# Kernel tuning notes

Hardware: AMD Instinct MI355X
Metric: run time of the kernel (lower is better)

Reference implementation:

```python
import jax, jax.numpy as jnp
import numpy as np

B, S, H = 2, 2048, 4096
NH, NKV, D = 32, 8, 128  # heads, kv heads, head_dim


def rotate_half(x):
    x1, x2 = jnp.split(x, 2, axis=-1)
    return jnp.concatenate((-x2, x1), axis=-1)


def setup_inputs() -> dict:
    key = jax.random.key(0)
    ks = jax.random.split(key, 5)
    hidden_states = jax.random.normal(ks[0], (B, S, H), jnp.float32) * 0.02
    wq = jax.random.normal(ks[1], (H, NH * D), jnp.float32) * 0.02
    wk = jax.random.normal(ks[2], (H, NKV * D), jnp.float32) * 0.02
    wv = jax.random.normal(ks[3], (H, NKV * D), jnp.float32) * 0.02
    wo = jax.random.normal(ks[4], (NH * D, H), jnp.float32) * 0.02
    # Llama rotary cache: emb = cat(freqs, freqs); cos/sin shape [S, D]
    inv_freq = 1.0 / (10000.0 ** (jnp.arange(0, D, 2, dtype=jnp.float32) / D))
    t = jnp.arange(S, dtype=jnp.float32)
    freqs = jnp.einsum('i,j->ij', t, inv_freq)
    emb = jnp.concatenate((freqs, freqs), axis=-1)
    cos, sin = jnp.cos(emb), jnp.sin(emb)
    # additive causal mask [S, S]
    causal = jnp.tril(jnp.ones((S, S), dtype=bool))
    attn_mask = jnp.where(causal, 0.0, -1e9).astype(jnp.float32)
    return {'hidden_states': hidden_states, 'wq': wq, 'wk': wk, 'wv': wv,
            'wo': wo, 'cos': cos, 'sin': sin, 'attn_mask': attn_mask}


def reference(hidden_states, wq, wk, wv, wo, cos, sin, attn_mask):
    b, s, _ = hidden_states.shape
    q = (hidden_states @ wq).reshape(b, s, NH, D)   # [b,s,nh,d]
    k = (hidden_states @ wk).reshape(b, s, NKV, D)  # [b,s,nkv,d]
    v = (hidden_states @ wv).reshape(b, s, NKV, D)
    c = cos[None, :, None, :]  # [1,s,1,d]
    sn = sin[None, :, None, :]
    q = q * c + rotate_half(q) * sn
    k = k * c + rotate_half(k) * sn
    # GQA: repeat KV heads to match query heads
    grp = NH // NKV
    k = jnp.repeat(k, grp, axis=2)
    v = jnp.repeat(v, grp, axis=2)
    scale = 1.0 / np.sqrt(D).astype(np.float32)
    scores = jnp.einsum('bqhd,bkhd->bhqk', q, k) * scale
    scores = scores + attn_mask[None, None, :, :]
    probs = jax.nn.softmax(scores, axis=-1)
    out = jnp.einsum('bhqk,bkhd->bqhd', probs, v).reshape(b, s, NH * D)
    return out @ wo
```

## Files before the change

kernel.cpp:

```cpp
#include <hip/hip_runtime.h>

typedef __attribute__((ext_vector_type(8))) short short8;
typedef __attribute__((ext_vector_type(4))) float f32x4;
typedef __attribute__((ext_vector_type(4))) int int4v;

__device__ __forceinline__ float bf2f(unsigned short u) {
  unsigned int x = ((unsigned int)u) << 16;
  float f;
  __builtin_memcpy(&f, &x, 4);
  return f;
}
__device__ __forceinline__ unsigned short f2bf(float f) {
  unsigned int x;
  __builtin_memcpy(&x, &f, 4);
  unsigned int r = (x + 0x7FFFu + ((x >> 16) & 1u)) >> 16;
  return (unsigned short)r;
}
__device__ __forceinline__ unsigned int cvtpk_bf16(float lo, float hi) {
  unsigned int r;
  asm("v_cvt_pk_bf16_f32 %0, %1, %2" : "=v"(r) : "v"(lo), "v"(hi));
  return r;
}
__device__ __forceinline__ int4v s8_to_i4(short8 v) {
  int4v r;
  __builtin_memcpy(&r, &v, 16);
  return r;
}
__device__ __forceinline__ short8 i4_to_s8(int4v v) {
  short8 r;
  __builtin_memcpy(&r, &v, 16);
  return r;
}
__device__ __forceinline__ short8 ld8_f32(const float* p) {
  f32x4 x = *(const f32x4*)p;
  f32x4 y = *(const f32x4*)(p + 4);
  short8 r;
  r[0] = (short)f2bf(x[0]); r[1] = (short)f2bf(x[1]);
  r[2] = (short)f2bf(x[2]); r[3] = (short)f2bf(x[3]);
  r[4] = (short)f2bf(y[0]); r[5] = (short)f2bf(y[1]);
  r[6] = (short)f2bf(y[2]); r[7] = (short)f2bf(y[3]);
  return r;
}

__device__ __forceinline__ void async16(unsigned short* lds, const unsigned short* g) {
  __builtin_amdgcn_global_load_lds(
      (const __attribute__((address_space(1))) void*)g,
      (__attribute__((address_space(3))) void*)lds, 16, 0, 0);
}

__global__ void downcast_f2b(const float* __restrict__ in,
                             unsigned short* __restrict__ out, int n8) {
  int i = blockIdx.x * 256 + threadIdx.x;
  if (i >= n8) return;
  *(short8*)(out + (size_t)i * 8) = ld8_f32(in + (size_t)i * 8);
}

__global__ void transpose_f2b(const float* __restrict__ in,
                              unsigned short* __restrict__ out, int R, int Ccols) {
  __shared__ unsigned short tile[32][33];
  const int c0 = blockIdx.x * 32;
  const int r0 = blockIdx.y * 32;
  const int tx = threadIdx.x, ty = threadIdx.y;
#pragma unroll
  for (int i = 0; i < 32; i += 8)
    tile[ty + i][tx] = f2bf(in[(size_t)(r0 + ty + i) * Ccols + (c0 + tx)]);
  __syncthreads();
#pragma unroll
  for (int i = 0; i < 32; i += 8)
    out[(size_t)(c0 + ty + i) * R + (r0 + tx)] = tile[tx][ty + i];
}

template <int CF32>
__global__ __launch_bounds__(256, 2) void gemm_bt(
    const unsigned short* __restrict__ A, const unsigned short* __restrict__ BT,
    void* __restrict__ Cp, int M, int N, int K) {
  alignas(16) __shared__ unsigned short lA[128 * 32];
  alignas(16) __shared__ unsigned short lB[128 * 32];
  const int tid = threadIdx.x;
  const int lane = tid & 63;
  const int wid = tid >> 6;
  const int wr = wid >> 1, wc = wid & 1;
  const int bm = blockIdx.x * 128;
  const int bn = blockIdx.y * 128;

  const int ar = tid >> 2;
  const int ac = (tid & 3) << 3;
  const unsigned short* aS0 = A + (size_t)(bm + ar) * K + ac;
  const unsigned short* aS1 = A + (size_t)(bm + 64 + ar) * K + ac;
  const unsigned short* bS0 = BT + (size_t)(bn + ar) * K + ac;
  const unsigned short* bS1 = BT + (size_t)(bn + 64 + ar) * K + ac;
  unsigned short* dA0 = lA + tid * 8;
  unsigned short* dA1 = lA + 2048 + tid * 8;
  unsigned short* dB0 = lB + tid * 8;
  unsigned short* dB1 = lB + 2048 + tid * 8;

  const int fr = lane & 15;
  const int fk = (lane >> 4) << 3;

  f32x4 acc[4][4] = {};

  for (int kt = 0; kt < K; kt += 32) {
    async16(dA0, aS0 + kt);
    async16(dA1, aS1 + kt);
    async16(dB0, bS0 + kt);
    async16(dB1, bS1 + kt);
    __syncthreads();
    short8 af[4], bfr[4];
#pragma unroll
    for (int i = 0; i < 4; i++) {
      af[i] = *(const short8*)(lA + (wr * 64 + i * 16 + fr) * 32 + fk);
      bfr[i] = *(const short8*)(lB + (wc * 64 + i * 16 + fr) * 32 + fk);
    }
#pragma unroll
    for (int i = 0; i < 4; i++)
#pragma unroll
      for (int j = 0; j < 4; j++)
        acc[i][j] = __builtin_amdgcn_mfma_f32_16x16x32_bf16(af[i], bfr[j], acc[i][j], 0, 0, 0);
    __syncthreads();
  }

  const int er = (lane >> 4) << 2;
#pragma unroll
  for (int i = 0; i < 4; i++) {
#pragma unroll
    for (int j = 0; j < 4; j++) {
      int row = bm + wr * 64 + i * 16 + er;
      int col = bn + wc * 64 + j * 16 + fr;
#pragma unroll
      for (int r = 0; r < 4; r++) {
        if constexpr (CF32)
          ((float*)Cp)[(size_t)(row + r) * N + col] = acc[i][j][r];
        else
          ((unsigned short*)Cp)[(size_t)(row + r) * N + col] = f2bf(acc[i][j][r]);
      }
    }
  }
}

__global__ void rope_kernel(unsigned short* __restrict__ buf,
                            const float* __restrict__ cosb,
                            const float* __restrict__ sinb,
                            int nh_shift, int rstride, int total) {
  int gid = blockIdx.x * 256 + threadIdx.x;
  if (gid >= total) return;
  int dblk = gid & 7;
  int u = gid >> 3;
  int head = u & ((1 << nh_shift) - 1);
  int token = u >> nh_shift;
  int s = token & 2047;
  int d0 = dblk << 3;
  unsigned short* p0 = buf + (size_t)token * rstride + (head << 7) + d0;
  unsigned short* p1 = p0 + 64;
  const float* cp = cosb + s * 128 + d0;
  const float* sp = sinb + s * 128 + d0;
  short8 a = *(const short8*)p0;
  short8 bq = *(const short8*)p1;
  f32x4 c0 = *(const f32x4*)cp, c1 = *(const f32x4*)(cp + 4);
  f32x4 s0 = *(const f32x4*)sp, s1 = *(const f32x4*)(sp + 4);
  short8 o0, o1;
#pragma unroll
  for (int j = 0; j < 8; j++) {
    float x0 = bf2f((unsigned short)a[j]);
    float x1 = bf2f((unsigned short)bq[j]);
    float c = (j < 4) ? c0[j & 3] : c1[j & 3];
    float sn = (j < 4) ? s0[j & 3] : s1[j & 3];
    o0[j] = (short)f2bf(x0 * c - x1 * sn);
    o1[j] = (short)f2bf(x1 * c + x0 * sn);
  }
  *(short8*)p0 = o0;
  *(short8*)p1 = o1;
}

#define LKD 136
#define LVW 36
#define ATT_SCALE 0.08838834764831845f
#define NEGBIG -30000.0f

__global__ __launch_bounds__(256, 2) void flash_attn(
    const unsigned short* __restrict__ Q, const unsigned short* __restrict__ KV,
    unsigned short* __restrict__ O) {
  alignas(16) __shared__ unsigned short lK[64 * LKD];
  alignas(16) __shared__ unsigned int lV[128 * LVW];

  const int tid = threadIdx.x;
  const int lane = tid & 63;
  const int w = tid >> 6;
  const int b = blockIdx.z;
  const int h = blockIdx.y;
  const int xa = blockIdx.x;
  const int kvh = h >> 2;

  const int fr = lane & 15;
  const int hi = lane >> 4;
  const int fk8 = hi << 3;
  const int hi4 = hi << 2;

  const int srow = tid >> 4;
  const int sc8 = (tid & 15) << 3;
  const int parity = srow & 1;

  const unsigned short* Kbp = KV + (size_t)(b * 2048) * 2048 + kvh * 128;
  const unsigned short* Vbp = Kbp + 1024;

  for (int pass = 0; pass < 2; pass++) {
    const int x = pass ? (15 - xa) : xa;
    const int q0 = x * 128;
    const int nt = 2 * x + 2;

    short8 qf[2][4];
#pragma unroll
    for (int qsub = 0; qsub < 2; qsub++) {
      const unsigned short* qb =
          Q + (size_t)(b * 2048 + q0 + w * 32 + qsub * 16 + fr) * 4096 + h * 128 + fk8;
#pragma unroll
      for (int ks = 0; ks < 4; ks++) qf[qsub][ks] = *(const short8*)(qb + ks * 32);
    }

    f32x4 oacc[2][8] = {};
    float m2[2] = {NEGBIG, NEGBIG};
    float ls[2] = {0.f, 0.f};

    short8 kreg[4], vreg[4];
#pragma unroll
    for (int rep = 0; rep < 4; rep++) {
      kreg[rep] = *(const short8*)(Kbp + (size_t)(rep * 16 + srow) * 2048 + sc8);
      vreg[rep] = *(const short8*)(Vbp + (size_t)(rep * 16 + srow) * 2048 + sc8);
    }

    for (int t = 0; t < nt; t++) {
      __syncthreads();
#pragma unroll
      for (int rep = 0; rep < 4; rep++)
        *(short8*)(lK + (rep * 16 + srow) * LKD + sc8) = kreg[rep];
#pragma unroll
      for (int rep = 0; rep < 4; rep++) {
        int4v own = s8_to_i4(vreg[rep]);
        int4v oth;
#pragma unroll
        for (int q = 0; q < 4; q++) oth[q] = __shfl_xor(own[q], 16);
        unsigned int oA = parity ? (unsigned)own[2] : (unsigned)own[0];
        unsigned int oB = parity ? (unsigned)own[3] : (unsigned)own[1];
        unsigned int tA = parity ? (unsigned)oth[2] : (unsigned)oth[0];
        unsigned int tB = parity ? (unsigned)oth[3] : (unsigned)oth[1];
        unsigned int evA = parity ? tA : oA, odA = parity ? oA : tA;
        unsigned int evB = parity ? tB : oB, odB = parity ? oB : tB;
        int d0 = sc8 + (parity << 2);
        int kvp = rep * 8 + (srow >> 1);
        lV[(d0 + 0) * LVW + kvp] = (evA & 0xFFFFu) | (odA << 16);
        lV[(d0 + 1) * LVW + kvp] = (evA >> 16) | (odA & 0xFFFF0000u);
        lV[(d0 + 2) * LVW + kvp] = (evB & 0xFFFFu) | (odB << 16);
        lV[(d0 + 3) * LVW + kvp] = (evB >> 16) | (odB & 0xFFFF0000u);
      }
      __syncthreads();

      if (t + 1 < nt) {
        const int kv1 = (t + 1) * 64;
#pragma unroll
        for (int rep = 0; rep < 4; rep++) {
          kreg[rep] = *(const short8*)(Kbp + (size_t)(kv1 + rep * 16 + srow) * 2048 + sc8);
          vreg[rep] = *(const short8*)(Vbp + (size_t)(kv1 + rep * 16 + srow) * 2048 + sc8);
        }
      }

      f32x4 sacc[2][4] = {};
      __builtin_amdgcn_s_setprio(1);
#pragma unroll
      for (int fc = 0; fc < 4; fc++)
#pragma unroll
        for (int ks = 0; ks < 4; ks++) {
          short8 bk = *(const short8*)(lK + (fc * 16 + fr) * LKD + ks * 32 + fk8);
          sacc[0][fc] = __builtin_amdgcn_mfma_f32_16x16x32_bf16(bk, qf[0][ks], sacc[0][fc], 0, 0, 0);
          sacc[1][fc] = __builtin_amdgcn_mfma_f32_16x16x32_bf16(bk, qf[1][ks], sacc[1][fc], 0, 0, 0);
        }
      __builtin_amdgcn_s_setprio(0);

      const bool diag = (t >= nt - 2);
      const int kvb = t * 64;
      unsigned int pk[2][4][2];

#pragma unroll
      for (int qsub = 0; qsub < 2; qsub++) {
        const int q = q0 + w * 32 + qsub * 16 + fr;
        float sv[4][4];
#pragma unroll
        for (int fc = 0; fc < 4; fc++)
#pragma unroll
          for (int r = 0; r < 4; r++) {
            float xx = sacc[qsub][fc][r] * ATT_SCALE;
            if (diag && (kvb + fc * 16 + hi4 + r > q)) xx = NEGBIG;
            sv[fc][r] = xx;
          }
        float mx = sv[0][0];
#pragma unroll
        for (int fc = 0; fc < 4; fc++)
#pragma unroll
          for (int r = 0; r < 4; r++) mx = fmaxf(mx, sv[fc][r]);
        mx = fmaxf(mx, __shfl_xor(mx, 16));
        mx = fmaxf(mx, __shfl_xor(mx, 32));
        float mnew = fmaxf(m2[qsub], mx);
        float alpha = __expf(m2[qsub] - mnew);
        m2[qsub] = mnew;
        float rs = 0.f;
        float p[4][4];
#pragma unroll
        for (int fc = 0; fc < 4; fc++)
#pragma unroll
          for (int r = 0; r < 4; r++) {
            p[fc][r] = __expf(sv[fc][r] - mnew);
            rs += p[fc][r];
          }
        rs += __shfl_xor(rs, 16);
        rs += __shfl_xor(rs, 32);
        ls[qsub] = ls[qsub] * alpha + rs;
#pragma unroll
        for (int fc = 0; fc < 4; fc++) {
          pk[qsub][fc][0] = cvtpk_bf16(p[fc][0], p[fc][1]);
          pk[qsub][fc][1] = cvtpk_bf16(p[fc][2], p[fc][3]);
        }
        f32x4 av;
#pragma unroll
        for (int r = 0; r < 4; r++) av[r] = __shfl(alpha, hi4 + r);
#pragma unroll
        for (int nf = 0; nf < 8; nf++) oacc[qsub][nf] *= av;
      }

      const int src0 = fr + ((hi & 1) << 5);
      const int src1 = src0 + 16;
#pragma unroll
      for (int kvs = 0; kvs < 2; kvs++) {
        unsigned int aw[2][4];
#pragma unroll
        for (int qsub = 0; qsub < 2; qsub++) {
#pragma unroll
          for (int jj = 0; jj < 4; jj++) {
            int src = (jj < 2) ? src0 : src1;
            int rr = jj & 1;
            unsigned int y0 = (unsigned)__shfl((int)pk[qsub][kvs * 2][rr], src);
            unsigned int y1 = (unsigned)__shfl((int)pk[qsub][kvs * 2 + 1][rr], src);
            aw[qsub][jj] = (hi >> 1) ? y1 : y0;
          }
        }
        int4v a0i = {(int)aw[0][0], (int)aw[0][1], (int)aw[0][2], (int)aw[0][3]};
        int4v a1i = {(int)aw[1][0], (int)aw[1][1], (int)aw[1][2], (int)aw[1][3]};
        short8 af0 = i4_to_s8(a0i), af1 = i4_to_s8(a1i);
        __builtin_amdgcn_s_setprio(1);
#pragma unroll
        for (int nf = 0; nf < 8; nf++) {
          int4v bvw = *(const int4v*)(lV + (nf * 16 + fr) * LVW + kvs * 16 + hi4);
          short8 bv = i4_to_s8(bvw);
          oacc[0][nf] = __builtin_amdgcn_mfma_f32_16x16x32_bf16(af0, bv, oacc[0][nf], 0, 0, 0);
          oacc[1][nf] = __builtin_amdgcn_mfma_f32_16x16x32_bf16(af1, bv, oacc[1][nf], 0, 0, 0);
        }
        __builtin_amdgcn_s_setprio(0);
      }
    }

#pragma unroll
    for (int qsub = 0; qsub < 2; qsub++) {
      f32x4 iv;
#pragma unroll
      for (int r = 0; r < 4; r++) iv[r] = 1.0f / __shfl(ls[qsub], hi4 + r);
#pragma unroll
      for (int r = 0; r < 4; r++) {
        unsigned short* op =
            O + (size_t)(b * 2048 + q0 + w * 32 + qsub * 16 + hi4 + r) * 4096 + h * 128 + fr;
#pragma unroll
        for (int nf = 0; nf < 8; nf++) op[nf * 16] = f2bf(oacc[qsub][nf][r] * iv[r]);
      }
    }
  }
}

extern "C" void kernel_launch(void* const* d_in, const int* in_sizes, int n_in,
                              void* d_out, int out_size, void* d_ws, size_t ws_size,
                              hipStream_t stream) {
  const float* hs = (const float*)d_in[0];
  const float* wq = (const float*)d_in[1];
  const float* wk = (const float*)d_in[2];
  const float* wv = (const float*)d_in[3];
  const float* wo = (const float*)d_in[4];
  const float* cosb = (const float*)d_in[5];
  const float* sinb = (const float*)d_in[6];

  unsigned short* ws = (unsigned short*)d_ws;
  unsigned short* T1 = ws;
  unsigned short* T2 = T1 + 16777216;
  unsigned short* T3 = T2 + 4194304;
  unsigned short* Qb = T3 + 4194304;
  unsigned short* KVb = Qb + 16777216;
  unsigned short* Ob = KVb + 8388608;

  unsigned short* hsb = (unsigned short*)d_out;

  dim3 tb(32, 8);
  downcast_f2b<<<8192, 256, 0, stream>>>(hs, hsb, 2097152);
  transpose_f2b<<<dim3(128, 128), tb, 0, stream>>>(wq, T1, 4096, 4096);
  transpose_f2b<<<dim3(32, 128), tb, 0, stream>>>(wk, T2, 4096, 1024);
  transpose_f2b<<<dim3(32, 128), tb, 0, stream>>>(wv, T3, 4096, 1024);

  gemm_bt<0><<<dim3(32, 32), 256, 0, stream>>>(hsb, T1, Qb, 4096, 4096, 4096);
  gemm_bt<0><<<dim3(32, 16), 256, 0, stream>>>(hsb, T2, KVb, 4096, 2048, 4096);

  transpose_f2b<<<dim3(128, 128), tb, 0, stream>>>(wo, T1, 4096, 4096);

  rope_kernel<<<4096, 256, 0, stream>>>(Qb, cosb, sinb, 5, 4096, 4096 * 32 * 8);
  rope_kernel<<<1024, 256, 0, stream>>>(KVb, cosb, sinb, 3, 2048, 4096 * 8 * 8);

  flash_attn<<<dim3(8, 32, 2), 256, 0, stream>>>(Qb, KVb, Ob);

  gemm_bt<1><<<dim3(32, 32), 256, 0, stream>>>(Ob, T1, (float*)d_out, 4096, 4096, 4096);
}
```

Before: 642.2 us.

## Use 256x256 double-buffered swizzled GEMM and XOR-swizzle attention LDS layouts

Replaces the 128x128 single-buffered GEMM with a 256x256-tile, 512-thread kernel that double-buffers LDS, prefetches two K-steps ahead with async loads, and XOR-swizzles LDS columns to avoid bank conflicts. It also replaces the padded K/V shared-memory layouts in flash attention with XOR swizzles. Larger tiles raise data reuse and cut global traffic, but the 4096x4096 GEMMs now launch only 256 blocks (128 for the KV GEMM), which may underfill the GPU, and register pressure rises from the 8x4 accumulator array.

```diff
diff --git a/kernel.cpp b/kernel.cpp
--- a/kernel.cpp
+++ b/kernel.cpp
@@ -71,67 +71,99 @@
 }
 
 template <int CF32>
-__global__ __launch_bounds__(256, 2) void gemm_bt(
+__global__ __launch_bounds__(512, 2) void gemm256(
     const unsigned short* __restrict__ A, const unsigned short* __restrict__ BT,
     void* __restrict__ Cp, int M, int N, int K) {
-  alignas(16) __shared__ unsigned short lA[128 * 32];
-  alignas(16) __shared__ unsigned short lB[128 * 32];
+  alignas(16) __shared__ unsigned short lA[2][256 * 32];
+  alignas(16) __shared__ unsigned short lB[2][256 * 32];
   const int tid = threadIdx.x;
-  const int lane = tid & 63;
-  const int wid = tid >> 6;
-  const int wr = wid >> 1, wc = wid & 1;
-  const int bm = blockIdx.x * 128;
-  const int bn = blockIdx.y * 128;
-
-  const int ar = tid >> 2;
-  const int ac = (tid & 3) << 3;
-  const unsigned short* aS0 = A + (size_t)(bm + ar) * K + ac;
-  const unsigned short* aS1 = A + (size_t)(bm + 64 + ar) * K + ac;
-  const unsigned short* bS0 = BT + (size_t)(bn + ar) * K + ac;
-  const unsigned short* bS1 = BT + (size_t)(bn + 64 + ar) * K + ac;
-  unsigned short* dA0 = lA + tid * 8;
-  unsigned short* dA1 = lA + 2048 + tid * 8;
-  unsigned short* dB0 = lB + tid * 8;
-  unsigned short* dB1 = lB + 2048 + tid * 8;
-
-  const int fr = lane & 15;
-  const int fk = (lane >> 4) << 3;
-
-  f32x4 acc[4][4] = {};
-
-  for (int kt = 0; kt < K; kt += 32) {
-    async16(dA0, aS0 + kt);
-    async16(dA1, aS1 + kt);
-    async16(dB0, bS0 + kt);
-    async16(dB1, bS1 + kt);
-    __syncthreads();
-    short8 af[4], bfr[4];
-#pragma unroll
-    for (int i = 0; i < 4; i++) {
-      af[i] = *(const short8*)(lA + (wr * 64 + i * 16 + fr) * 32 + fk);
-      bfr[i] = *(const short8*)(lB + (wc * 64 + i * 16 + fr) * 32 + fk);
-    }
-#pragma unroll
-    for (int i = 0; i < 4; i++)
-#pragma unroll
-      for (int j = 0; j < 4; j++)
-        acc[i][j] = __builtin_amdgcn_mfma_f32_16x16x32_bf16(af[i], bfr[j], acc[i][j], 0, 0, 0);
-    __syncthreads();
+  const int l = tid & 63;
+  const int wv = tid >> 6;
+  const int wr = wv >> 2;
+  const int wc = wv & 3;
+  const int bm = blockIdx.x * 256;
+  const int bn = blockIdx.y * 256;
+
+  const int scol = (((l & 3) ^ ((l >> 3) & 3)) << 3);
+  const int r0c = (wv * 2) * 16 + (l >> 2);
+  const unsigned short* aS0 = A + (size_t)(bm + r0c) * K + scol;
+  const unsigned short* aS1 = A + (size_t)(bm + r0c + 16) * K + scol;
+  const unsigned short* bS0 = BT + (size_t)(bn + r0c) * K + scol;
+  const unsigned short* bS1 = BT + (size_t)(bn + r0c + 16) * K + scol;
+  const int dOf0 = (wv * 2) * 512 + l * 8;
+  const int dOf1 = (wv * 2 + 1) * 512 + l * 8;
+
+  const int fr = l & 15;
+  const int hi = l >> 4;
+  const int coff = (hi * 8) ^ (((fr >> 1) & 3) << 3);
+
+  f32x4 acc[8][4] = {};
+  const int nt = K >> 5;
+
+#pragma unroll
+  for (int bufi = 0; bufi < 2; bufi++) {
+    if (bufi < nt) {
+      const int kt = bufi * 32;
+      async16(&lA[bufi][dOf0], aS0 + kt);
+      async16(&lA[bufi][dOf1], aS1 + kt);
+      async16(&lB[bufi][dOf0], bS0 + kt);
+      async16(&lB[bufi][dOf1], bS1 + kt);
+    }
   }
-
-  const int er = (lane >> 4) << 2;
-#pragma unroll
-  for (int i = 0; i < 4; i++) {
-#pragma unroll
-    for (int j = 0; j < 4; j++) {
-      int row = bm + wr * 64 + i * 16 + er;
-      int col = bn + wc * 64 + j * 16 + fr;
+  if (nt > 1)
+    asm volatile("s_waitcnt vmcnt(4)" ::: "memory");
+  else
+    asm volatile("s_waitcnt vmcnt(0)" ::: "memory");
+  __builtin_amdgcn_sched_barrier(0);
+  asm volatile("s_barrier" ::: "memory");
+
+  for (int t = 0; t < nt; ++t) {
+    const int cur = t & 1;
+    short8 a[8], b[4];
+#pragma unroll
+    for (int mi = 0; mi < 8; mi++) {
+      int row = wr * 128 + mi * 16 + fr;
+      a[mi] = *(const short8*)(&lA[cur][row * 32 + coff]);
+    }
+#pragma unroll
+    for (int ni = 0; ni < 4; ni++) {
+      int row = wc * 64 + ni * 16 + fr;
+      b[ni] = *(const short8*)(&lB[cur][row * 32 + coff]);
+    }
+    __builtin_amdgcn_s_setprio(1);
+#pragma unroll
+    for (int mi = 0; mi < 8; mi++)
+#pragma unroll
+      for (int ni = 0; ni < 4; ni++)
+        acc[mi][ni] = __builtin_amdgcn_mfma_f32_16x16x32_bf16(a[mi], b[ni], acc[mi][ni], 0, 0, 0);
+    __builtin_amdgcn_s_setprio(0);
+    asm volatile("s_barrier" ::: "memory");
+    if (t + 2 < nt) {
+      const int kt = (t + 2) * 32;
+      async16(&lA[cur][dOf0], aS0 + kt);
+      async16(&lA[cur][dOf1], aS1 + kt);
+      async16(&lB[cur][dOf0], bS0 + kt);
+      async16(&lB[cur][dOf1], bS1 + kt);
+      asm volatile("s_waitcnt vmcnt(4)" ::: "memory");
+    } else {
+      asm volatile("s_waitcnt vmcnt(0)" ::: "memory");
+    }
+    __builtin_amdgcn_sched_barrier(0);
+    asm volatile("s_barrier" ::: "memory");
+  }
+
+#pragma unroll
+  for (int mi = 0; mi < 8; mi++) {
+#pragma unroll
+    for (int ni = 0; ni < 4; ni++) {
+      int row = bm + wr * 128 + mi * 16 + hi * 4;
+      int col = bn + wc * 64 + ni * 16 + fr;
 #pragma unroll
       for (int r = 0; r < 4; r++) {
         if constexpr (CF32)
-          ((float*)Cp)[(size_t)(row + r) * N + col] = acc[i][j][r];
+          ((float*)Cp)[(size_t)(row + r) * N + col] = acc[mi][ni][r];
         else
-          ((unsigned short*)Cp)[(size_t)(row + r) * N + col] = f2bf(acc[i][j][r]);
+          ((unsigned short*)Cp)[(size_t)(row + r) * N + col] = f2bf(acc[mi][ni][r]);
       }
     }
   }
@@ -171,16 +203,16 @@
   *(short8*)p1 = o1;
 }
 
-#define LKD 136
-#define LVW 36
 #define ATT_SCALE 0.08838834764831845f
 #define NEGBIG -30000.0f
+
+__device__ __forceinline__ int vswz(int d) { return (((d >> 3) ^ d) & 7) << 2; }
 
 __global__ __launch_bounds__(256, 2) void flash_attn(
     const unsigned short* __restrict__ Q, const unsigned short* __restrict__ KV,
     unsigned short* __restrict__ O) {
-  alignas(16) __shared__ unsigned short lK[64 * LKD];
-  alignas(16) __shared__ unsigned int lV[128 * LVW];
+  alignas(16) __shared__ unsigned short lK[64 * 128];
+  alignas(16) __shared__ unsigned int lV[128 * 32];
 
   const int tid = threadIdx.x;
   const int lane = tid & 63;
@@ -231,7 +263,7 @@
       __syncthreads();
 #pragma unroll
       for (int rep = 0; rep < 4; rep++)
-        *(short8*)(lK + (rep * 16 + srow) * LKD + sc8) = kreg[rep];
+        *(short8*)(lK + (rep * 16 + srow) * 128 + (sc8 ^ ((srow & 7) << 3))) = kreg[rep];
 #pragma unroll
       for (int rep = 0; rep < 4; rep++) {
         int4v own = s8_to_i4(vreg[rep]);
@@ -246,10 +278,10 @@
         unsigned int evB = parity ? tB : oB, odB = parity ? oB : tB;
         int d0 = sc8 + (parity << 2);
         int kvp = rep * 8 + (srow >> 1);
-        lV[(d0 + 0) * LVW + kvp] = (evA & 0xFFFFu) | (odA << 16);
-        lV[(d0 + 1) * LVW + kvp] = (evA >> 16) | (odA & 0xFFFF0000u);
-        lV[(d0 + 2) * LVW + kvp] = (evB & 0xFFFFu) | (odB << 16);
-        lV[(d0 + 3) * LVW + kvp] = (evB >> 16) | (odB & 0xFFFF0000u);
+        lV[(d0 + 0) * 32 + (kvp ^ vswz(d0 + 0))] = (evA & 0xFFFFu) | (odA << 16);
+        lV[(d0 + 1) * 32 + (kvp ^ vswz(d0 + 1))] = (evA >> 16) | (odA & 0xFFFF0000u);
+        lV[(d0 + 2) * 32 + (kvp ^ vswz(d0 + 2))] = (evB & 0xFFFFu) | (odB << 16);
+        lV[(d0 + 3) * 32 + (kvp ^ vswz(d0 + 3))] = (evB >> 16) | (odB & 0xFFFF0000u);
       }
       __syncthreads();
 
@@ -268,7 +300,8 @@
       for (int fc = 0; fc < 4; fc++)
 #pragma unroll
         for (int ks = 0; ks < 4; ks++) {
-          short8 bk = *(const short8*)(lK + (fc * 16 + fr) * LKD + ks * 32 + fk8);
+          short8 bk = *(const short8*)(lK + (fc * 16 + fr) * 128 +
+                                       ((ks * 32 + fk8) ^ ((fr & 7) << 3)));
           sacc[0][fc] = __builtin_amdgcn_mfma_f32_16x16x32_bf16(bk, qf[0][ks], sacc[0][fc], 0, 0, 0);
           sacc[1][fc] = __builtin_amdgcn_mfma_f32_16x16x32_bf16(bk, qf[1][ks], sacc[1][fc], 0, 0, 0);
         }
@@ -346,7 +379,8 @@
         __builtin_amdgcn_s_setprio(1);
 #pragma unroll
         for (int nf = 0; nf < 8; nf++) {
-          int4v bvw = *(const int4v*)(lV + (nf * 16 + fr) * LVW + kvs * 16 + hi4);
+          int row = nf * 16 + fr;
+          int4v bvw = *(const int4v*)(lV + row * 32 + ((kvs * 16 + hi4) ^ vswz(row)));
           short8 bv = i4_to_s8(bvw);
           oacc[0][nf] = __builtin_amdgcn_mfma_f32_16x16x32_bf16(af0, bv, oacc[0][nf], 0, 0, 0);
           oacc[1][nf] = __builtin_amdgcn_mfma_f32_16x16x32_bf16(af1, bv, oacc[1][nf], 0, 0, 0);
@@ -398,8 +432,8 @@
   transpose_f2b<<<dim3(32, 128), tb, 0, stream>>>(wk, T2, 4096, 1024);
   transpose_f2b<<<dim3(32, 128), tb, 0, stream>>>(wv, T3, 4096, 1024);
 
-  gemm_bt<0><<<dim3(32, 32), 256, 0, stream>>>(hsb, T1, Qb, 4096, 4096, 4096);
-  gemm_bt<0><<<dim3(32, 16), 256, 0, stream>>>(hsb, T2, KVb, 4096, 2048, 4096);
+  gemm256<0><<<dim3(16, 16), 512, 0, stream>>>(hsb, T1, Qb, 4096, 4096, 4096);
+  gemm256<0><<<dim3(16, 8), 512, 0, stream>>>(hsb, T2, KVb, 4096, 2048, 4096);
 
   transpose_f2b<<<dim3(128, 128), tb, 0, stream>>>(wo, T1, 4096, 4096);
 
@@ -408,5 +442,5 @@
 
   flash_attn<<<dim3(8, 32, 2), 256, 0, stream>>>(Qb, KVb, Ob);
 
-  gemm_bt<1><<<dim3(32, 32), 256, 0, stream>>>(Ob, T1, (float*)d_out, 4096, 4096, 4096);
-}
+  gemm256<1><<<dim3(16, 16), 512, 0, stream>>>(Ob, T1, (float*)d_out, 4096, 4096, 4096);
+}
```

Result: slower. 684.5 us (+6.6%).
